# Kernel optimization log

Measured on AMD Instinct MI355X. Metric: run time of the kernel, lower is better.

## Reference

```python
import jax, jax.numpy as jnp
import numpy as np

B, T = 128, 2048
N_VIS, N_HID, N_REC = 88, 150, 100

def setup_inputs() -> dict:
    key = jax.random.key(0)
    ks = jax.random.split(key, 6)
    padded = (jax.random.uniform(ks[0], (B, T, N_VIS)) < 0.12).astype(jnp.float32)  # sparse binary piano roll
    mask = jnp.ones((B, T), dtype=jnp.float32)
    lstm_shifted = jax.random.normal(ks[1], (B, T, N_REC), dtype=jnp.float32)
    W = jax.random.normal(ks[2], (N_VIS, N_HID), dtype=jnp.float32) * 0.01
    bv = jnp.zeros((N_VIS,), dtype=jnp.float32)
    bh = jnp.zeros((N_HID,), dtype=jnp.float32)
    Wyv = jax.random.normal(ks[3], (N_VIS, N_REC), dtype=jnp.float32) * 1e-4  # nn.Linear weight [out,in]
    Wyh = jax.random.normal(ks[4], (N_HID, N_REC), dtype=jnp.float32) * 1e-4
    return {"padded": padded, "mask": mask, "lstm_shifted": lstm_shifted,
            "W": W, "bv": bv, "bh": bh, "Wyv": Wyv, "Wyh": Wyh, "k": 5}


def reference(padded, mask, lstm_shifted, W, bv, bh, Wyv, Wyh, k):
    # Time-dependent biases: bv_t [B,T,88], bh_t [B,T,150]
    bv_t = bv + jnp.einsum('btr,vr->btv', lstm_shifted, Wyv)
    bh_t = bh + jnp.einsum('btr,hr->bth', lstm_shifted, Wyh)

    rng = jax.random.key(42)
    v_sample = padded
    mean_v = None
    for i in range(k):  # CD-k Gibbs chain (k is a static Python int)
        kh, kv = jax.random.split(jax.random.fold_in(rng, i))
        mean_h = jax.nn.sigmoid(v_sample @ W + bh_t)                       # [B,T,150]
        h = (jax.random.uniform(kh, mean_h.shape) < mean_h).astype(padded.dtype)
        mean_v = jax.nn.sigmoid(h @ W.T + bv_t)                            # [B,T,88]
        v_sample = (jax.random.uniform(kv, mean_v.shape) < mean_v).astype(padded.dtype)

    def free_energy(v):  # [B,T]
        return -(v * bv_t).sum(-1) - jax.nn.softplus(v @ W + bh_t).sum(-1)

    msum = mask.sum()
    cost = ((free_energy(padded) - free_energy(jax.lax.stop_gradient(v_sample))) * mask).sum() / msum
    eps = 1e-10
    ll = (padded * jnp.log(mean_v + eps) + (1.0 - padded) * jnp.log(1.0 - mean_v + eps)).sum(-1)
    monitor = (ll * mask).sum() / msum
    return cost, monitor
```

## Files before the change

### kernel.cpp

```cpp
#include <hip/hip_runtime.h>
#include <stdint.h>


#define NV 88
#define NH 150
#define NR 100
#define NBT (128*2048)
#define CPB 32
#define NBLK (NBT/CPB)

#define WSTR 168
#define TSTR 104
#define HSTR 168
#define VSTR 104
#define LSTR 136

#define OFF_WL    0
#define OFF_WT    16128
#define OFF_H     31936
#define OFF_V     37312
#define OFF_REDC  40640
#define SMEM_SZ   40896
#define OFF_LS    0

#define WSF_BYTES (NBLK*3*4)
#define TAB_WL    0
#define TAB_WT    16128
#define TAB_YH    31936
#define TAB_YV    53696
#define TAB_BYTES 66752

typedef float f32x4 __attribute__((ext_vector_type(4)));

#define SCHED_FENCE() __builtin_amdgcn_sched_barrier(0)

__device__ __forceinline__ uint32_t hashu(uint32_t x) {
  x *= 0x9E3779B9u;
  x ^= x >> 16;
  x *= 0x85EBCA6Bu;
  x ^= x >> 16;
  return x;
}

__device__ __forceinline__ uint8_t f2e4m3(float x) {
  uint8_t s = (uint8_t)((__float_as_uint(x) >> 24) & 0x80u);
  float a = fabsf(x);
  if (!(a < 448.0f)) a = 448.0f;
  if (a < 0.015625f) {
    int mi = (int)rintf(a * 512.0f);
    return s | (uint8_t)mi;
  }
  uint32_t u = __float_as_uint(a);
  u += 0x7FFFFu + ((u >> 20) & 1u);
  int e = (int)(u >> 23) - 127;
  uint32_t mm = (u >> 20) & 7u;
  return s | (uint8_t)(((e + 7) << 3) | mm);
}

__global__ void rbm_prep(const float* __restrict__ W,  const float* __restrict__ bv,
                         const float* __restrict__ bh, const float* __restrict__ Wyv,
                         const float* __restrict__ Wyh, uint8_t* __restrict__ tab)
{
  for (int i = blockIdx.x*256 + threadIdx.x; i < TAB_BYTES; i += gridDim.x*256) {
    uint8_t v = 0;
    if (i < TAB_WT) {
      int r = i / WSTR, c = i - r*WSTR;
      if (r < NV && c < NH) v = f2e4m3(W[r*NH + c] * 16.0f);
    } else if (i < TAB_YH) {
      int j = i - TAB_WT;
      int r = j / TSTR, c = j - r*TSTR;
      if (r < NH && c < NV) v = f2e4m3(W[c*NH + r] * 16.0f);
    } else if (i < TAB_YV) {
      int j = i - TAB_YH;
      int r = j / LSTR, c = j - r*LSTR;
      if (r < NH) { if (c < NR) v = f2e4m3(Wyh[r*NR + c]*256.0f);
                    else if (c == NR) v = f2e4m3(bh[r]*256.0f); }
    } else {
      int j = i - TAB_YV;
      int r = j / LSTR, c = j - r*LSTR;
      if (r < NV) { if (c < NR) v = f2e4m3(Wyv[r*NR + c]*256.0f);
                    else if (c == NR) v = f2e4m3(bv[r]*256.0f); }
    }
    tab[i] = v;
  }
}

__global__ __launch_bounds__(256, 4) void rbm_cdk_mfma(
    const float* __restrict__ padded, const float* __restrict__ mask,
    const float* __restrict__ lstm,   const uint8_t* __restrict__ tab,
    const int*  __restrict__ kptr,    float* __restrict__ wsf)
{
  __shared__ __align__(16) unsigned char smem[SMEM_SZ];
  uint8_t*  Wl   = (uint8_t*)(smem + OFF_WL);
  uint8_t*  WTl  = (uint8_t*)(smem + OFF_WT);
  uint8_t*  Hl   = (uint8_t*)(smem + OFF_H);
  uint8_t*  Vl   = (uint8_t*)(smem + OFF_V);
  float*    redc = (float*)  (smem + OFF_REDC);
  uint8_t*  Ls   = (uint8_t*)(smem + OFF_LS);

  const int tid = threadIdx.x;
  const int l   = tid & 63;
  const int w   = tid >> 6;
  const int nc  = w >> 1;
  const int h   = w & 1;
  const int Cb  = blockIdx.x * CPB;
  const int k   = kptr[0];

  const int col = l & 15;
  const int g   = l >> 4;
  const int kb8 = g * 8;
  const int chain = 16*nc + col;
  const int Cg    = Cb + chain;

  for (int i = tid; i < CPB*LSTR; i += 256) {
    int r = i / LSTR, c = i - r*LSTR;
    uint8_t v = 0;
    if (c < NR) v = f2e4m3(lstm[(size_t)(Cb + r)*NR + c] * 0.0625f);
    else if (c == NR) v = 0x18;
    Ls[i] = v;
  }
  for (int i = tid; i < CPB*VSTR; i += 256) {
    int r = i / VSTR, c = i - r*VSTR;
    uint8_t v = 0;
    if (c < NV) v = (padded[(size_t)(Cb + r)*NV + c] > 0.5f) ? 0x18 : 0;
    Vl[i] = v;
  }
  {
    uint32_t* H32 = (uint32_t*)Hl;
    for (int i = tid; i < CPB*HSTR/4; i += 256) H32[i] = 0;
  }
  __syncthreads();

  f32x4 bhF[5], bvF[3];
  {
    const uint8_t* Yhg = tab + TAB_YH;
    const uint8_t* Yvg = tab + TAB_YV;
    long bl[4];
    #pragma unroll
    for (int ks = 0; ks < 4; ++ks)
      bl[ks] = *(const long*)(Ls + chain*LSTR + kb8 + 32*ks);
    #pragma unroll
    for (int ni = 0; ni < 5; ++ni) {
      const int n = h*5 + ni;
      f32x4 acc = {0.f, 0.f, 0.f, 0.f};
      #pragma unroll
      for (int ks = 0; ks < 4; ++ks) {
        long a = *(const long*)(Yhg + (size_t)(16*n + col)*LSTR + kb8 + 32*ks);
        acc = __builtin_amdgcn_mfma_f32_16x16x32_fp8_fp8(a, bl[ks], acc, 0, 0, 0);
      }
      #pragma unroll
      for (int r = 0; r < 4; ++r) acc[r] *= 0.0625f;
      bhF[ni] = acc;
      SCHED_FENCE();
    }
    #pragma unroll
    for (int ni = 0; ni < 3; ++ni) {
      const int n = h*3 + ni;
      f32x4 acc = {0.f, 0.f, 0.f, 0.f};
      #pragma unroll
      for (int ks = 0; ks < 4; ++ks) {
        long a = *(const long*)(Yvg + (size_t)(16*n + col)*LSTR + kb8 + 32*ks);
        acc = __builtin_amdgcn_mfma_f32_16x16x32_fp8_fp8(a, bl[ks], acc, 0, 0, 0);
      }
      #pragma unroll
      for (int r = 0; r < 4; ++r) acc[r] *= 0.0625f;
      bvF[ni] = acc;
      SCHED_FENCE();
    }
  }
  __syncthreads();

  {
    const uint4* src = (const uint4*)tab;
    uint4* dst = (uint4*)smem;
    for (int i = tid; i < 31936/16; i += 256) dst[i] = src[i];
  }
  uint32_t pbits = 0;
  #pragma unroll
  for (int ni = 0; ni < 3; ++ni) {
    const int vb = 16*(h*3 + ni) + 4*g;
    if (vb < NV) {
      const uint32_t wd = *(const uint32_t*)(Vl + chain*VSTR + vb);
      #pragma unroll
      for (int r = 0; r < 4; ++r)
        if ((wd >> (8*r)) & 0xFFu) pbits |= 1u << (4*ni + r);
    }
  }
  __syncthreads();

  float spd = 0.0f, llv = 0.0f, dd = 0.0f;

  auto hidden = [&](int t, bool firstSP) {
    long bfrag[3];
    #pragma unroll
    for (int ks = 0; ks < 3; ++ks)
      bfrag[ks] = *(const long*)(Vl + chain*VSTR + kb8 + 32*ks);
    const uint32_t sbase = (uint32_t)Cg | ((uint32_t)t << 25);
    #pragma unroll
    for (int ni = 0; ni < 5; ++ni) {
      const int n = h*5 + ni;
      f32x4 acc = bhF[ni];
      #pragma unroll
      for (int ks = 0; ks < 3; ++ks) {
        long a = *(const long*)(WTl + (size_t)(16*n + col)*TSTR + kb8 + 32*ks);
        acc = __builtin_amdgcn_mfma_f32_16x16x32_fp8_fp8(a, bfrag[ks], acc, 0, 0, 0);
      }
      const int jb = 16*n + 4*g;
      const int nreal = NH - jb;
      uint32_t word = 0;
      #pragma unroll
      for (int p = 0; p < 2; ++p) {
        const float pre0 = acc[2*p], pre1 = acc[2*p+1];
        const float e0 = __expf(-pre0), e1 = __expf(-pre1);
        if (firstSP) {
          if (2*p   < nreal) spd -= pre0 + __logf(1.0f + e0);
          if (2*p+1 < nreal) spd -= pre1 + __logf(1.0f + e1);
        }
        const uint32_t x = hashu(sbase + ((uint32_t)((jb >> 1) + p) << 18));
        const float u0 = (float)(x & 0xFFFFu);
        const float u1 = (float)(x >> 16);
        const bool b0 = (2*p   < nreal) && (fmaf(u0, e0, u0) < 65536.0f);
        const bool b1 = (2*p+1 < nreal) && (fmaf(u1, e1, u1) < 65536.0f);
        word |= (b0 ? 0x18u : 0u) << (16*p);
        word |= (b1 ? 0x18u : 0u) << (16*p + 8);
      }
      if (jb < NH)
        *(uint32_t*)(Hl + chain*HSTR + jb) = word;
      SCHED_FENCE();
    }
  };

  auto visible = [&](int t, bool lastLL) {
    long bfrag[5];
    #pragma unroll
    for (int ks = 0; ks < 5; ++ks)
      bfrag[ks] = *(const long*)(Hl + chain*HSTR + kb8 + 32*ks);
    const uint32_t sbase = (uint32_t)Cg | ((uint32_t)t << 25) | (1u << 28);
    #pragma unroll
    for (int ni = 0; ni < 3; ++ni) {
      const int n = h*3 + ni;
      f32x4 acc = bvF[ni];
      #pragma unroll
      for (int ks = 0; ks < 5; ++ks) {
        long a = *(const long*)(Wl + (size_t)(16*n + col)*WSTR + kb8 + 32*ks);
        acc = __builtin_amdgcn_mfma_f32_16x16x32_fp8_fp8(a, bfrag[ks], acc, 0, 0, 0);
      }
      const int vb = 16*n + 4*g;
      const bool real = (vb < NV);
      uint32_t word = 0;
      #pragma unroll
      for (int p = 0; p < 2; ++p) {
        const float pre0 = acc[2*p], pre1 = acc[2*p+1];
        const float e0 = __expf(-pre0), e1 = __expf(-pre1);
        const uint32_t x = hashu(sbase + ((uint32_t)((vb >> 1) + p) << 18));
        const float u0 = (float)(x & 0xFFFFu);
        const float u1 = (float)(x >> 16);
        const bool b0 = real && (fmaf(u0, e0, u0) < 65536.0f);
        const bool b1 = real && (fmaf(u1, e1, u1) < 65536.0f);
        if (lastLL && real) {
          const float L0 = __logf(1.0f + e0), L1 = __logf(1.0f + e1);
          const uint32_t pb0 = (pbits >> (4*ni + 2*p))     & 1u;
          const uint32_t pb1 = (pbits >> (4*ni + 2*p + 1)) & 1u;
          llv += -L0 - (pb0 ? 0.0f : pre0);
          llv += -L1 - (pb1 ? 0.0f : pre1);
          const float bvt0 = bvF[ni][2*p], bvt1 = bvF[ni][2*p+1];
          dd += (b0 ? bvt0 : 0.0f) - (pb0 ? bvt0 : 0.0f);
          dd += (b1 ? bvt1 : 0.0f) - (pb1 ? bvt1 : 0.0f);
        }
        word |= (b0 ? 0x18u : 0u) << (16*p);
        word |= (b1 ? 0x18u : 0u) << (16*p + 8);
      }
      if (real)
        *(uint32_t*)(Vl + chain*VSTR + vb) = word;
      SCHED_FENCE();
    }
  };

  auto finalsp = [&]() {
    long bfrag[3];
    #pragma unroll
    for (int ks = 0; ks < 3; ++ks)
      bfrag[ks] = *(const long*)(Vl + chain*VSTR + kb8 + 32*ks);
    #pragma unroll
    for (int ni = 0; ni < 5; ++ni) {
      const int n = h*5 + ni;
      f32x4 acc = bhF[ni];
      #pragma unroll
      for (int ks = 0; ks < 3; ++ks) {
        long a = *(const long*)(WTl + (size_t)(16*n + col)*TSTR + kb8 + 32*ks);
        acc = __builtin_amdgcn_mfma_f32_16x16x32_fp8_fp8(a, bfrag[ks], acc, 0, 0, 0);
      }
      const int jb = 16*n + 4*g;
      const int nreal = NH - jb;
      #pragma unroll
      for (int r = 0; r < 4; ++r) {
        if (r < nreal) {
          const float e = __expf(-acc[r]);
          spd += acc[r] + __logf(1.0f + e);
        }
      }
      SCHED_FENCE();
    }
  };

  hidden(0, true);
  __syncthreads();
  for (int t = 0; t < k - 1; ++t) {
    visible(t, false);
    __syncthreads();
    hidden(t + 1, false);
    __syncthreads();
  }
  visible(k - 1, true);
  __syncthreads();
  finalsp();

  float ca = dd + spd;
  ca  += __shfl_xor(ca, 16);  ca  += __shfl_xor(ca, 32);
  llv += __shfl_xor(llv, 16); llv += __shfl_xor(llv, 32);
  if (l < 16 && h == 0) { redc[chain*2] = ca; redc[chain*2+1] = llv; }
  __syncthreads();
  if (l < 16 && h == 1) { redc[chain*2] += ca; redc[chain*2+1] += llv; }
  __syncthreads();
  if (tid < CPB) {
    const float mk = mask[Cb + tid];
    float aa = redc[tid*2]   * mk;
    float bb = redc[tid*2+1] * mk;
    float mm = mk;
    #pragma unroll
    for (int off = 1; off <= 16; off <<= 1) {
      aa += __shfl_xor(aa, off);
      bb += __shfl_xor(bb, off);
      mm += __shfl_xor(mm, off);
    }
    if (tid == 0) {
      wsf[(size_t)blockIdx.x*3+0] = aa;
      wsf[(size_t)blockIdx.x*3+1] = bb;
      wsf[(size_t)blockIdx.x*3+2] = mm;
    }
  }
}

__global__ void rbm_finalize_kernel(const float* __restrict__ wsf, float* __restrict__ out)
{
  __shared__ double sh[3][4];
  const int tid = threadIdx.x, lane = tid & 63, w = tid >> 6;
  double sa = 0.0, sb = 0.0, sm = 0.0;
  for (int i = tid; i < NBLK; i += 256) {
    sa += (double)wsf[(size_t)3*i+0];
    sb += (double)wsf[(size_t)3*i+1];
    sm += (double)wsf[(size_t)3*i+2];
  }
  #pragma unroll
  for (int off = 32; off >= 1; off >>= 1) {
    sa += __shfl_down(sa, off);
    sb += __shfl_down(sb, off);
    sm += __shfl_down(sm, off);
  }
  if (lane == 0) { sh[0][w] = sa; sh[1][w] = sb; sh[2][w] = sm; }
  __syncthreads();
  if (tid == 0) {
    double A = sh[0][0]+sh[0][1]+sh[0][2]+sh[0][3];
    double B = sh[1][0]+sh[1][1]+sh[1][2]+sh[1][3];
    double M = sh[2][0]+sh[2][1]+sh[2][2]+sh[2][3];
    out[0] = (float)(A / M);
    out[1] = (float)(B / M);
  }
}

extern "C" void kernel_launch(void* const* d_in, const int* in_sizes, int n_in,
                              void* d_out, int out_size, void* d_ws, size_t ws_size,
                              hipStream_t stream) {
  const float* padded = (const float*)d_in[0];
  const float* mask   = (const float*)d_in[1];
  const float* lstm   = (const float*)d_in[2];
  const float* W      = (const float*)d_in[3];
  const float* bv     = (const float*)d_in[4];
  const float* bh     = (const float*)d_in[5];
  const float* Wyv    = (const float*)d_in[6];
  const float* Wyh    = (const float*)d_in[7];
  const int*   kp     = (const int*)d_in[8];
  float*   wsf = (float*)d_ws;
  uint8_t* tab = (uint8_t*)d_ws + WSF_BYTES;
  float*   out = (float*)d_out;

  rbm_prep<<<264, 256, 0, stream>>>(W, bv, bh, Wyv, Wyh, tab);
  rbm_cdk_mfma<<<NBLK, 256, 0, stream>>>(padded, mask, lstm, tab, kp, wsf);
  rbm_finalize_kernel<<<1, 256, 0, stream>>>(wsf, out);
}
```

Baseline: 291.3 us.

## Split each chain group's output tiles across four waves instead of two

Doubles the block to 512 threads so four waves, instead of two, share the hidden and visible output tiles of each 16-chain group. Tiles are interleaved across waves (n = h + 4*ni), which cuts per-wave serial MFMA and transcendental work and register use. The aim is to shorten the latency of each Gibbs step and hide more of it with extra waves. In exchange it adds uneven tile counts per wave (3/2 vs 2/1), more block-wide barriers in the final reduction, and more threads waiting at each __syncthreads.

```diff
diff --git a/kernel.cpp b/kernel.cpp
--- a/kernel.cpp
+++ b/kernel.cpp
@@ -85,7 +85,7 @@
   }
 }
 
-__global__ __launch_bounds__(256, 4) void rbm_cdk_mfma(
+__global__ __launch_bounds__(512, 6) void rbm_cdk_mfma(
     const float* __restrict__ padded, const float* __restrict__ mask,
     const float* __restrict__ lstm,   const uint8_t* __restrict__ tab,
     const int*  __restrict__ kptr,    float* __restrict__ wsf)
@@ -101,10 +101,13 @@
   const int tid = threadIdx.x;
   const int l   = tid & 63;
   const int w   = tid >> 6;
-  const int nc  = w >> 1;
-  const int h   = w & 1;
+  const int nc  = w >> 2;
+  const int h   = w & 3;
   const int Cb  = blockIdx.x * CPB;
   const int k   = kptr[0];
+
+  const int NTH = (h < 2) ? 3 : 2;
+  const int NTV = (h < 2) ? 2 : 1;
 
   const int col = l & 15;
   const int g   = l >> 4;
@@ -112,14 +115,14 @@
   const int chain = 16*nc + col;
   const int Cg    = Cb + chain;
 
-  for (int i = tid; i < CPB*LSTR; i += 256) {
+  for (int i = tid; i < CPB*LSTR; i += 512) {
     int r = i / LSTR, c = i - r*LSTR;
     uint8_t v = 0;
     if (c < NR) v = f2e4m3(lstm[(size_t)(Cb + r)*NR + c] * 0.0625f);
     else if (c == NR) v = 0x18;
     Ls[i] = v;
   }
-  for (int i = tid; i < CPB*VSTR; i += 256) {
+  for (int i = tid; i < CPB*VSTR; i += 512) {
     int r = i / VSTR, c = i - r*VSTR;
     uint8_t v = 0;
     if (c < NV) v = (padded[(size_t)(Cb + r)*NV + c] > 0.5f) ? 0x18 : 0;
@@ -127,11 +130,11 @@
   }
   {
     uint32_t* H32 = (uint32_t*)Hl;
-    for (int i = tid; i < CPB*HSTR/4; i += 256) H32[i] = 0;
-  }
-  __syncthreads();
-
-  f32x4 bhF[5], bvF[3];
+    for (int i = tid; i < CPB*HSTR/4; i += 512) H32[i] = 0;
+  }
+  __syncthreads();
+
+  f32x4 bhF[3], bvF[2];
   {
     const uint8_t* Yhg = tab + TAB_YH;
     const uint8_t* Yvg = tab + TAB_YV;
@@ -140,32 +143,36 @@
     for (int ks = 0; ks < 4; ++ks)
       bl[ks] = *(const long*)(Ls + chain*LSTR + kb8 + 32*ks);
     #pragma unroll
-    for (int ni = 0; ni < 5; ++ni) {
-      const int n = h*5 + ni;
-      f32x4 acc = {0.f, 0.f, 0.f, 0.f};
-      #pragma unroll
-      for (int ks = 0; ks < 4; ++ks) {
-        long a = *(const long*)(Yhg + (size_t)(16*n + col)*LSTR + kb8 + 32*ks);
-        acc = __builtin_amdgcn_mfma_f32_16x16x32_fp8_fp8(a, bl[ks], acc, 0, 0, 0);
-      }
-      #pragma unroll
-      for (int r = 0; r < 4; ++r) acc[r] *= 0.0625f;
-      bhF[ni] = acc;
-      SCHED_FENCE();
-    }
-    #pragma unroll
     for (int ni = 0; ni < 3; ++ni) {
-      const int n = h*3 + ni;
-      f32x4 acc = {0.f, 0.f, 0.f, 0.f};
-      #pragma unroll
-      for (int ks = 0; ks < 4; ++ks) {
-        long a = *(const long*)(Yvg + (size_t)(16*n + col)*LSTR + kb8 + 32*ks);
-        acc = __builtin_amdgcn_mfma_f32_16x16x32_fp8_fp8(a, bl[ks], acc, 0, 0, 0);
-      }
-      #pragma unroll
-      for (int r = 0; r < 4; ++r) acc[r] *= 0.0625f;
-      bvF[ni] = acc;
-      SCHED_FENCE();
+      if (ni < NTH) {
+        const int n = h + 4*ni;
+        f32x4 acc = {0.f, 0.f, 0.f, 0.f};
+        #pragma unroll
+        for (int ks = 0; ks < 4; ++ks) {
+          long a = *(const long*)(Yhg + (size_t)(16*n + col)*LSTR + kb8 + 32*ks);
+          acc = __builtin_amdgcn_mfma_f32_16x16x32_fp8_fp8(a, bl[ks], acc, 0, 0, 0);
+        }
+        #pragma unroll
+        for (int r = 0; r < 4; ++r) acc[r] *= 0.0625f;
+        bhF[ni] = acc;
+        SCHED_FENCE();
+      }
+    }
+    #pragma unroll
+    for (int ni = 0; ni < 2; ++ni) {
+      if (ni < NTV) {
+        const int n = h + 4*ni;
+        f32x4 acc = {0.f, 0.f, 0.f, 0.f};
+        #pragma unroll
+        for (int ks = 0; ks < 4; ++ks) {
+          long a = *(const long*)(Yvg + (size_t)(16*n + col)*LSTR + kb8 + 32*ks);
+          acc = __builtin_amdgcn_mfma_f32_16x16x32_fp8_fp8(a, bl[ks], acc, 0, 0, 0);
+        }
+        #pragma unroll
+        for (int r = 0; r < 4; ++r) acc[r] *= 0.0625f;
+        bvF[ni] = acc;
+        SCHED_FENCE();
+      }
     }
   }
   __syncthreads();
@@ -173,17 +180,19 @@
   {
     const uint4* src = (const uint4*)tab;
     uint4* dst = (uint4*)smem;
-    for (int i = tid; i < 31936/16; i += 256) dst[i] = src[i];
+    for (int i = tid; i < 31936/16; i += 512) dst[i] = src[i];
   }
   uint32_t pbits = 0;
   #pragma unroll
-  for (int ni = 0; ni < 3; ++ni) {
-    const int vb = 16*(h*3 + ni) + 4*g;
-    if (vb < NV) {
-      const uint32_t wd = *(const uint32_t*)(Vl + chain*VSTR + vb);
-      #pragma unroll
-      for (int r = 0; r < 4; ++r)
-        if ((wd >> (8*r)) & 0xFFu) pbits |= 1u << (4*ni + r);
+  for (int ni = 0; ni < 2; ++ni) {
+    if (ni < NTV) {
+      const int vb = 16*(h + 4*ni) + 4*g;
+      if (vb < NV) {
+        const uint32_t wd = *(const uint32_t*)(Vl + chain*VSTR + vb);
+        #pragma unroll
+        for (int r = 0; r < 4; ++r)
+          if ((wd >> (8*r)) & 0xFFu) pbits |= 1u << (4*ni + r);
+      }
     }
   }
   __syncthreads();
@@ -197,36 +206,38 @@
       bfrag[ks] = *(const long*)(Vl + chain*VSTR + kb8 + 32*ks);
     const uint32_t sbase = (uint32_t)Cg | ((uint32_t)t << 25);
     #pragma unroll
-    for (int ni = 0; ni < 5; ++ni) {
-      const int n = h*5 + ni;
-      f32x4 acc = bhF[ni];
-      #pragma unroll
-      for (int ks = 0; ks < 3; ++ks) {
-        long a = *(const long*)(WTl + (size_t)(16*n + col)*TSTR + kb8 + 32*ks);
-        acc = __builtin_amdgcn_mfma_f32_16x16x32_fp8_fp8(a, bfrag[ks], acc, 0, 0, 0);
-      }
-      const int jb = 16*n + 4*g;
-      const int nreal = NH - jb;
-      uint32_t word = 0;
-      #pragma unroll
-      for (int p = 0; p < 2; ++p) {
-        const float pre0 = acc[2*p], pre1 = acc[2*p+1];
-        const float e0 = __expf(-pre0), e1 = __expf(-pre1);
-        if (firstSP) {
-          if (2*p   < nreal) spd -= pre0 + __logf(1.0f + e0);
-          if (2*p+1 < nreal) spd -= pre1 + __logf(1.0f + e1);
-        }
-        const uint32_t x = hashu(sbase + ((uint32_t)((jb >> 1) + p) << 18));
-        const float u0 = (float)(x & 0xFFFFu);
-        const float u1 = (float)(x >> 16);
-        const bool b0 = (2*p   < nreal) && (fmaf(u0, e0, u0) < 65536.0f);
-        const bool b1 = (2*p+1 < nreal) && (fmaf(u1, e1, u1) < 65536.0f);
-        word |= (b0 ? 0x18u : 0u) << (16*p);
-        word |= (b1 ? 0x18u : 0u) << (16*p + 8);
-      }
-      if (jb < NH)
-        *(uint32_t*)(Hl + chain*HSTR + jb) = word;
-      SCHED_FENCE();
+    for (int ni = 0; ni < 3; ++ni) {
+      if (ni < NTH) {
+        const int n = h + 4*ni;
+        f32x4 acc = bhF[ni];
+        #pragma unroll
+        for (int ks = 0; ks < 3; ++ks) {
+          long a = *(const long*)(WTl + (size_t)(16*n + col)*TSTR + kb8 + 32*ks);
+          acc = __builtin_amdgcn_mfma_f32_16x16x32_fp8_fp8(a, bfrag[ks], acc, 0, 0, 0);
+        }
+        const int jb = 16*n + 4*g;
+        const int nreal = NH - jb;
+        uint32_t word = 0;
+        #pragma unroll
+        for (int p = 0; p < 2; ++p) {
+          const float pre0 = acc[2*p], pre1 = acc[2*p+1];
+          const float e0 = __expf(-pre0), e1 = __expf(-pre1);
+          if (firstSP) {
+            if (2*p   < nreal) spd -= pre0 + __logf(1.0f + e0);
+            if (2*p+1 < nreal) spd -= pre1 + __logf(1.0f + e1);
+          }
+          const uint32_t x = hashu(sbase + ((uint32_t)((jb >> 1) + p) << 18));
+          const float u0 = (float)(x & 0xFFFFu);
+          const float u1 = (float)(x >> 16);
+          const bool b0 = (2*p   < nreal) && (fmaf(u0, e0, u0) < 65536.0f);
+          const bool b1 = (2*p+1 < nreal) && (fmaf(u1, e1, u1) < 65536.0f);
+          word |= (b0 ? 0x18u : 0u) << (16*p);
+          word |= (b1 ? 0x18u : 0u) << (16*p + 8);
+        }
+        if (jb < NH)
+          *(uint32_t*)(Hl + chain*HSTR + jb) = word;
+        SCHED_FENCE();
+      }
     }
   };
 
@@ -237,42 +248,44 @@
       bfrag[ks] = *(const long*)(Hl + chain*HSTR + kb8 + 32*ks);
     const uint32_t sbase = (uint32_t)Cg | ((uint32_t)t << 25) | (1u << 28);
     #pragma unroll
-    for (int ni = 0; ni < 3; ++ni) {
-      const int n = h*3 + ni;
-      f32x4 acc = bvF[ni];
-      #pragma unroll
-      for (int ks = 0; ks < 5; ++ks) {
-        long a = *(const long*)(Wl + (size_t)(16*n + col)*WSTR + kb8 + 32*ks);
-        acc = __builtin_amdgcn_mfma_f32_16x16x32_fp8_fp8(a, bfrag[ks], acc, 0, 0, 0);
-      }
-      const int vb = 16*n + 4*g;
-      const bool real = (vb < NV);
-      uint32_t word = 0;
-      #pragma unroll
-      for (int p = 0; p < 2; ++p) {
-        const float pre0 = acc[2*p], pre1 = acc[2*p+1];
-        const float e0 = __expf(-pre0), e1 = __expf(-pre1);
-        const uint32_t x = hashu(sbase + ((uint32_t)((vb >> 1) + p) << 18));
-        const float u0 = (float)(x & 0xFFFFu);
-        const float u1 = (float)(x >> 16);
-        const bool b0 = real && (fmaf(u0, e0, u0) < 65536.0f);
-        const bool b1 = real && (fmaf(u1, e1, u1) < 65536.0f);
-        if (lastLL && real) {
-          const float L0 = __logf(1.0f + e0), L1 = __logf(1.0f + e1);
-          const uint32_t pb0 = (pbits >> (4*ni + 2*p))     & 1u;
-          const uint32_t pb1 = (pbits >> (4*ni + 2*p + 1)) & 1u;
-          llv += -L0 - (pb0 ? 0.0f : pre0);
-          llv += -L1 - (pb1 ? 0.0f : pre1);
-          const float bvt0 = bvF[ni][2*p], bvt1 = bvF[ni][2*p+1];
-          dd += (b0 ? bvt0 : 0.0f) - (pb0 ? bvt0 : 0.0f);
-          dd += (b1 ? bvt1 : 0.0f) - (pb1 ? bvt1 : 0.0f);
-        }
-        word |= (b0 ? 0x18u : 0u) << (16*p);
-        word |= (b1 ? 0x18u : 0u) << (16*p + 8);
-      }
-      if (real)
-        *(uint32_t*)(Vl + chain*VSTR + vb) = word;
-      SCHED_FENCE();
+    for (int ni = 0; ni < 2; ++ni) {
+      if (ni < NTV) {
+        const int n = h + 4*ni;
+        f32x4 acc = bvF[ni];
+        #pragma unroll
+        for (int ks = 0; ks < 5; ++ks) {
+          long a = *(const long*)(Wl + (size_t)(16*n + col)*WSTR + kb8 + 32*ks);
+          acc = __builtin_amdgcn_mfma_f32_16x16x32_fp8_fp8(a, bfrag[ks], acc, 0, 0, 0);
+        }
+        const int vb = 16*n + 4*g;
+        const bool real = (vb < NV);
+        uint32_t word = 0;
+        #pragma unroll
+        for (int p = 0; p < 2; ++p) {
+          const float pre0 = acc[2*p], pre1 = acc[2*p+1];
+          const float e0 = __expf(-pre0), e1 = __expf(-pre1);
+          const uint32_t x = hashu(sbase + ((uint32_t)((vb >> 1) + p) << 18));
+          const float u0 = (float)(x & 0xFFFFu);
+          const float u1 = (float)(x >> 16);
+          const bool b0 = real && (fmaf(u0, e0, u0) < 65536.0f);
+          const bool b1 = real && (fmaf(u1, e1, u1) < 65536.0f);
+          if (lastLL && real) {
+            const float L0 = __logf(1.0f + e0), L1 = __logf(1.0f + e1);
+            const uint32_t pb0 = (pbits >> (4*ni + 2*p))     & 1u;
+            const uint32_t pb1 = (pbits >> (4*ni + 2*p + 1)) & 1u;
+            llv += -L0 - (pb0 ? 0.0f : pre0);
+            llv += -L1 - (pb1 ? 0.0f : pre1);
+            const float bvt0 = bvF[ni][2*p], bvt1 = bvF[ni][2*p+1];
+            dd += (b0 ? bvt0 : 0.0f) - (pb0 ? bvt0 : 0.0f);
+            dd += (b1 ? bvt1 : 0.0f) - (pb1 ? bvt1 : 0.0f);
+          }
+          word |= (b0 ? 0x18u : 0u) << (16*p);
+          word |= (b1 ? 0x18u : 0u) << (16*p + 8);
+        }
+        if (real)
+          *(uint32_t*)(Vl + chain*VSTR + vb) = word;
+        SCHED_FENCE();
+      }
     }
   };
 
@@ -282,24 +295,26 @@
     for (int ks = 0; ks < 3; ++ks)
       bfrag[ks] = *(const long*)(Vl + chain*VSTR + kb8 + 32*ks);
     #pragma unroll
-    for (int ni = 0; ni < 5; ++ni) {
-      const int n = h*5 + ni;
-      f32x4 acc = bhF[ni];
-      #pragma unroll
-      for (int ks = 0; ks < 3; ++ks) {
-        long a = *(const long*)(WTl + (size_t)(16*n + col)*TSTR + kb8 + 32*ks);
-        acc = __builtin_amdgcn_mfma_f32_16x16x32_fp8_fp8(a, bfrag[ks], acc, 0, 0, 0);
-      }
-      const int jb = 16*n + 4*g;
-      const int nreal = NH - jb;
-      #pragma unroll
-      for (int r = 0; r < 4; ++r) {
-        if (r < nreal) {
-          const float e = __expf(-acc[r]);
-          spd += acc[r] + __logf(1.0f + e);
-        }
-      }
-      SCHED_FENCE();
+    for (int ni = 0; ni < 3; ++ni) {
+      if (ni < NTH) {
+        const int n = h + 4*ni;
+        f32x4 acc = bhF[ni];
+        #pragma unroll
+        for (int ks = 0; ks < 3; ++ks) {
+          long a = *(const long*)(WTl + (size_t)(16*n + col)*TSTR + kb8 + 32*ks);
+          acc = __builtin_amdgcn_mfma_f32_16x16x32_fp8_fp8(a, bfrag[ks], acc, 0, 0, 0);
+        }
+        const int jb = 16*n + 4*g;
+        const int nreal = NH - jb;
+        #pragma unroll
+        for (int r = 0; r < 4; ++r) {
+          if (r < nreal) {
+            const float e = __expf(-acc[r]);
+            spd += acc[r] + __logf(1.0f + e);
+          }
+        }
+        SCHED_FENCE();
+      }
     }
   };
 
@@ -318,10 +333,14 @@
   float ca = dd + spd;
   ca  += __shfl_xor(ca, 16);  ca  += __shfl_xor(ca, 32);
   llv += __shfl_xor(llv, 16); llv += __shfl_xor(llv, 32);
-  if (l < 16 && h == 0) { redc[chain*2] = ca; redc[chain*2+1] = llv; }
-  __syncthreads();
-  if (l < 16 && h == 1) { redc[chain*2] += ca; redc[chain*2+1] += llv; }
-  __syncthreads();
+  #pragma unroll
+  for (int hp = 0; hp < 4; ++hp) {
+    if (h == hp && l < 16) {
+      if (hp == 0) { redc[chain*2] = ca;  redc[chain*2+1] = llv; }
+      else         { redc[chain*2] += ca; redc[chain*2+1] += llv; }
+    }
+    __syncthreads();
+  }
   if (tid < CPB) {
     const float mk = mask[Cb + tid];
     float aa = redc[tid*2]   * mk;
@@ -385,6 +404,6 @@
   float*   out = (float*)d_out;
 
   rbm_prep<<<264, 256, 0, stream>>>(W, bv, bh, Wyv, Wyh, tab);
-  rbm_cdk_mfma<<<NBLK, 256, 0, stream>>>(padded, mask, lstm, tab, kp, wsf);
+  rbm_cdk_mfma<<<NBLK, 512, 0, stream>>>(padded, mask, lstm, tab, kp, wsf);
   rbm_finalize_kernel<<<1, 256, 0, stream>>>(wsf, out);
 }
```

New measurement: 292.0 us. No clear change (+0.3%).
